# Kernel tuning notes

Hardware: AMD Instinct MI355X
Metric: run time of the kernel (lower is better)

The kernel has to match this reference:

```python
import jax, jax.numpy as jnp
import numpy as np

B = 8
IMG = 224; PATCH = 16; C_IN = 3
GRID = IMG // PATCH           # 14
NPATCH = GRID * GRID          # 196
D_MODEL = 768
N_LAYERS = 12
D_STATE = 16
D_CONV = 4
D_INNER = 2 * D_MODEL         # 1536
DT_RANK = 48                  # ceil(768/16)
MASK_RATIO = 0.25
LEN_KEEP = int(NPATCH * (1.0 - MASK_RATIO))  # 147


def _sincos_1d(dim, pos):
    omega = np.arange(dim // 2, dtype=np.float64) / (dim / 2.0)
    omega = 1.0 / (10000.0 ** omega)
    out = np.einsum('m,d->md', pos.reshape(-1).astype(np.float64), omega)
    return np.concatenate([np.sin(out), np.cos(out)], axis=1)


def get_2d_sincos_pos_embed(embed_dim, grid_size, add_cls_token=True):
    grid_h = np.arange(grid_size, dtype=np.float32)
    grid_w = np.arange(grid_size, dtype=np.float32)
    grid = np.meshgrid(grid_w, grid_h)
    grid = np.stack(grid, axis=0).reshape([2, 1, grid_size, grid_size])
    emb_h = _sincos_1d(embed_dim // 2, grid[0])
    emb_w = _sincos_1d(embed_dim // 2, grid[1])
    pos = np.concatenate([emb_h, emb_w], axis=1)
    if add_cls_token:
        pos = np.concatenate([np.zeros([1, embed_dim]), pos], axis=0)
    return pos.astype(np.float32)


def setup_inputs() -> dict:
    key = jax.random.key(0)
    ks = jax.random.split(key, 16)
    sc = 0.02
    pixel_values = jax.random.normal(ks[0], (B, C_IN, IMG, IMG), jnp.float32)
    noise = jax.random.uniform(ks[1], (B, NPATCH), jnp.float32)
    conv_w = jax.random.normal(ks[2], (D_MODEL, C_IN, PATCH, PATCH), jnp.float32) * sc
    conv_b = jnp.zeros((D_MODEL,), jnp.float32)
    cls_token = jax.random.normal(ks[3], (1, 1, D_MODEL), jnp.float32) * sc
    pos_embed = jnp.asarray(get_2d_sincos_pos_embed(D_MODEL, GRID, True))  # (197, 768)
    ln_w = jnp.ones((N_LAYERS, D_MODEL), jnp.float32)
    ln_b = jnp.zeros((N_LAYERS, D_MODEL), jnp.float32)
    W_in = jax.random.normal(ks[4], (N_LAYERS, 2 * D_INNER, D_MODEL), jnp.float32) * sc
    conv1d_w = jax.random.normal(ks[5], (N_LAYERS, D_INNER, D_CONV), jnp.float32) * sc
    conv1d_b = jnp.zeros((N_LAYERS, D_INNER), jnp.float32)
    W_x = jax.random.normal(ks[6], (N_LAYERS, DT_RANK + 2 * D_STATE, D_INNER), jnp.float32) * sc
    dt_std = DT_RANK ** (-0.5)
    W_dt = jax.random.uniform(ks[7], (N_LAYERS, D_INNER, DT_RANK), jnp.float32, -dt_std, dt_std)
    u = jax.random.uniform(ks[8], (N_LAYERS, D_INNER), jnp.float32)
    dt = jnp.exp(u * (np.log(0.1) - np.log(0.001)) + np.log(0.001))
    dt_bias = dt + jnp.log(-jnp.expm1(-dt))  # inverse softplus
    A_log = jnp.broadcast_to(jnp.log(jnp.arange(1, D_STATE + 1, dtype=jnp.float32)),
                             (N_LAYERS, D_INNER, D_STATE)).copy()
    Dp = jnp.ones((N_LAYERS, D_INNER), jnp.float32)
    W_out = jax.random.normal(ks[9], (N_LAYERS, D_MODEL, D_INNER), jnp.float32) * sc
    lnf_w = jnp.ones((D_MODEL,), jnp.float32)
    lnf_b = jnp.zeros((D_MODEL,), jnp.float32)
    return dict(pixel_values=pixel_values, noise=noise, conv_w=conv_w, conv_b=conv_b,
                cls_token=cls_token, pos_embed=pos_embed, ln_w=ln_w, ln_b=ln_b,
                W_in=W_in, conv1d_w=conv1d_w, conv1d_b=conv1d_b, W_x=W_x, W_dt=W_dt,
                dt_bias=dt_bias, A_log=A_log, Dp=Dp, W_out=W_out, lnf_w=lnf_w, lnf_b=lnf_b)


def layer_norm(x, w, b, eps=1e-12):
    mu = jnp.mean(x, axis=-1, keepdims=True)
    var = jnp.var(x, axis=-1, keepdims=True)
    return (x - mu) * jax.lax.rsqrt(var + eps) * w + b


def mamba_mixer(x, W_in, cw, cb, W_x, W_dt, dtb, A_log, Dp, W_out):
    # x: (B, L, D_MODEL)
    Bb, L, _ = x.shape
    xz = jnp.einsum('bld,ed->ble', x, W_in)           # (B, L, 2*d_inner)
    xs, z = jnp.split(xz, 2, axis=-1)
    # depthwise causal conv over time
    xc = xs.transpose(0, 2, 1)                        # (B, d_inner, L)
    xc = jax.lax.conv_general_dilated(xc, cw[:, None, :], (1,), [(D_CONV - 1, 0)],
                                      dimension_numbers=('NCH', 'OIH', 'NCH'),
                                      feature_group_count=D_INNER) + cb[None, :, None]
    xc = jax.nn.silu(xc).transpose(0, 2, 1)           # (B, L, d_inner)
    x_dbl = jnp.einsum('bld,rd->blr', xc, W_x)        # (B, L, dt_rank+2*d_state)
    dt, Bm, Cm = jnp.split(x_dbl, [DT_RANK, DT_RANK + D_STATE], axis=-1)
    dt = jax.nn.softplus(jnp.einsum('blr,dr->bld', dt, W_dt) + dtb)  # (B, L, d_inner)
    A = -jnp.exp(A_log)                               # (d_inner, d_state)
    dA = jnp.exp(dt[..., None] * A)                   # (B, L, d_inner, d_state)
    dBu = (dt * xc)[..., None] * Bm[:, :, None, :]    # (B, L, d_inner, d_state)

    def step(h, inp):
        dA_t, dBu_t, C_t = inp
        h = dA_t * h + dBu_t                          # (B, d_inner, d_state)
        y = jnp.einsum('bdn,bn->bd', h, C_t)
        return h, y

    h0 = jnp.zeros((Bb, D_INNER, D_STATE), xc.dtype)
    _, ys = jax.lax.scan(step, h0, (dA.transpose(1, 0, 2, 3), dBu.transpose(1, 0, 2, 3),
                                    Cm.transpose(1, 0, 2)))
    y = ys.transpose(1, 0, 2) + xc * Dp               # skip via D
    y = y * jax.nn.silu(z)                            # output gate
    return jnp.einsum('bld,od->blo', y, W_out)


def reference(pixel_values, noise, conv_w, conv_b, cls_token, pos_embed, ln_w, ln_b,
              W_in, conv1d_w, conv1d_b, W_x, W_dt, dt_bias, A_log, Dp, W_out, lnf_w, lnf_b):
    Bb = pixel_values.shape[0]
    # patch embedding (conv stride = patch)
    x = jax.lax.conv_general_dilated(pixel_values, conv_w, (PATCH, PATCH), 'VALID',
                                     dimension_numbers=('NCHW', 'OIHW', 'NCHW'))
    x = x.reshape(Bb, D_MODEL, NPATCH).transpose(0, 2, 1) + conv_b  # (B, 196, 768)
    x = x + pos_embed[1:][None]
    # random masking (noise supplied externally for determinism)
    ids_shuffle = jnp.argsort(noise, axis=1)
    ids_restore = jnp.argsort(ids_shuffle, axis=1)
    ids_keep = ids_shuffle[:, :LEN_KEEP]
    x = jnp.take_along_axis(x, ids_keep[:, :, None], axis=1)        # (B, 147, 768)
    mask = jnp.ones((Bb, NPATCH), jnp.float32).at[:, :LEN_KEEP].set(0.0)
    mask = jnp.take_along_axis(mask, ids_restore, axis=1)
    # prepend CLS
    cls = jnp.broadcast_to(cls_token + pos_embed[:1][None], (Bb, 1, D_MODEL))
    h = jnp.concatenate([cls, x], axis=1)                            # (B, 148, 768)

    def layer(hc, p):
        lw, lb, Wi, cw, cb, Wx, Wd, db, Al, Dd, Wo = p
        return hc + mamba_mixer(layer_norm(hc, lw, lb), Wi, cw, cb, Wx, Wd, db, Al, Dd, Wo), None

    h, _ = jax.lax.scan(layer, h, (ln_w, ln_b, W_in, conv1d_w, conv1d_b, W_x, W_dt,
                                   dt_bias, A_log, Dp, W_out))
    h = layer_norm(h, lnf_w, lnf_b)
    return h, mask, ids_restore
```

## Files before the change

### kernel.cpp

```cpp
#include <hip/hip_runtime.h>


#define BATCH 8
#define NPATCH 196
#define LEN_KEEP 147
#define SEQ 148
#define DM 768
#define DI 1536
#define DTR 48
#define DST 16
#define MTOK (BATCH*SEQ)
#define MT MTOK

typedef __bf16 bf16_t;
typedef bf16_t bf16x8 __attribute__((ext_vector_type(8)));
typedef float  f32x4  __attribute__((ext_vector_type(4)));
typedef unsigned short u16;
typedef u16 u16x8 __attribute__((ext_vector_type(8)));

__device__ __forceinline__ u16 f2bf(float f) {
    union { float f; unsigned u; } c; c.f = f;
    unsigned r = c.u + 0x7FFFu + ((c.u >> 16) & 1u);
    return (u16)(r >> 16);
}
__device__ __forceinline__ float bf2f(u16 u) {
    union { unsigned u; float f; } c; c.u = ((unsigned)u) << 16; return c.f;
}
__device__ __forceinline__ float sigmoidf_(float x) { return 1.f / (1.f + __expf(-x)); }

__device__ __forceinline__ void gl_lds16(const void* g, void* l) {
    __builtin_amdgcn_global_load_lds(
        (const __attribute__((address_space(1))) unsigned int*)g,
        (__attribute__((address_space(3))) unsigned int*)l, 16, 0, 0);
}

__global__ __launch_bounds__(256) void k_im2col(const float* __restrict__ px,
                                                u16* __restrict__ Ap) {
    int idx = blockIdx.x * 256 + threadIdx.x;
    if (idx >= 1568 * 192) return;
    int m = idx / 192, kq = (idx % 192) * 4;
    int b = m / NPATCH, p = m % NPATCH;
    int c = kq / 256, r = kq % 256, i = r / 16, j = r % 16;
    int y = (p / 14) * 16 + i, x = (p % 14) * 16 + j;
    float4 v = *reinterpret_cast<const float4*>(&px[((size_t)(b * 3 + c) * 224 + y) * 224 + x]);
    ushort4 w4 = { f2bf(v.x), f2bf(v.y), f2bf(v.z), f2bf(v.w) };
    *reinterpret_cast<ushort4*>(&Ap[(size_t)m * 768 + kq]) = w4;
}

__global__ __launch_bounds__(256) void k_mask(const float* __restrict__ noise,
                                              int* __restrict__ ids_shuf,
                                              float* __restrict__ out_mask,
                                              float* __restrict__ out_restore) {
    __shared__ float sn[NPATCH];
    __shared__ int sshuf[NPATCH];
    int b = blockIdx.x, tid = threadIdx.x;
    if (tid < NPATCH) sn[tid] = noise[b * NPATCH + tid];
    __syncthreads();
    if (tid < NPATCH) {
        float nj = sn[tid];
        int rank = 0;
        for (int i = 0; i < NPATCH; ++i) {
            float ni = sn[i];
            rank += (ni < nj) || (ni == nj && i < tid);
        }
        out_restore[b * NPATCH + tid] = (float)rank;
        out_mask[b * NPATCH + tid] = (rank >= LEN_KEEP) ? 1.f : 0.f;
        sshuf[rank] = tid;
    }
    __syncthreads();
    if (tid < NPATCH) ids_shuf[b * NPATCH + tid] = sshuf[tid];
}

__global__ __launch_bounds__(256) void k_build_h(const float* __restrict__ embed,
                                                 const int* __restrict__ ids_shuf,
                                                 const float* __restrict__ cls,
                                                 const float* __restrict__ pos,
                                                 float* __restrict__ h) {
    int blk = blockIdx.x;
    int b = blk / SEQ, t = blk % SEQ, tid = threadIdx.x;
    size_t ob = (size_t)blk * DM;
    if (t == 0) {
        for (int i = tid; i < DM; i += 256) h[ob + i] = cls[i] + pos[i];
    } else {
        int j = ids_shuf[b * NPATCH + (t - 1)];
        const float* src = embed + (size_t)(b * NPATCH + j) * DM;
        for (int i = tid; i < DM; i += 256) h[ob + i] = src[i];
    }
}

template <int OUT_BF>
__global__ __launch_bounds__(256) void k_layernorm(const float* __restrict__ in,
                                                   const float* __restrict__ w,
                                                   const float* __restrict__ b,
                                                   void* __restrict__ outv) {
    int row = blockIdx.x, tid = threadIdx.x;
    const float* x = in + (size_t)row * DM;
    float v0 = x[tid], v1 = x[tid + 256], v2 = x[tid + 512];
    float s = v0 + v1 + v2, q = v0 * v0 + v1 * v1 + v2 * v2;
#pragma unroll
    for (int off = 32; off; off >>= 1) {
        s += __shfl_down(s, off, 64);
        q += __shfl_down(q, off, 64);
    }
    __shared__ float ss[4], sq[4];
    int wid = tid >> 6, lane = tid & 63;
    if (lane == 0) { ss[wid] = s; sq[wid] = q; }
    __syncthreads();
    float st = ss[0] + ss[1] + ss[2] + ss[3];
    float qt = sq[0] + sq[1] + sq[2] + sq[3];
    float mu = st * (1.f / DM);
    float var = qt * (1.f / DM) - mu * mu;
    float rstd = rsqrtf(var + 1e-12f);
    float r0 = (v0 - mu) * rstd * w[tid]       + b[tid];
    float r1 = (v1 - mu) * rstd * w[tid + 256] + b[tid + 256];
    float r2 = (v2 - mu) * rstd * w[tid + 512] + b[tid + 512];
    if (OUT_BF) {
        u16* o = (u16*)outv + (size_t)row * DM;
        o[tid] = f2bf(r0); o[tid + 256] = f2bf(r1); o[tid + 512] = f2bf(r2);
    } else {
        float* o = (float*)outv + (size_t)row * DM;
        o[tid] = r0; o[tid + 256] = r1; o[tid + 512] = r2;
    }
}

template <int EPI>
__global__ __launch_bounds__(256) void gemm64(
    const u16* __restrict__ A, int lda, int M,
    const u16* __restrict__ B, int ldb, int N,
    void* __restrict__ Cv, int ldc, int kChunk,
    const float* __restrict__ e0, const float* __restrict__ e1) {
    __shared__ u16 sm[2][128 * 64];
    const int tid = threadIdx.x;
    const int m0 = blockIdx.x * 64, n0 = blockIdx.y * 64;
    const int kStart = blockIdx.z * kChunk;
    const int lane = tid & 63, wid = tid >> 6;
    const int wr = wid >> 1, wc = wid & 1;
    const int lr = lane & 15, lg = lane >> 4;
    const int subrow = lane >> 3, kpart = lane & 7;
    const int kel = 8 * (kpart ^ subrow);

    f32x4 acc[2][2] = {};
    const int nt = kChunk / 64;

    {
        const int k0 = kStart;
#pragma unroll
        for (int s = 0; s < 2; ++s) {
            int rb = wid * 16 + s * 8;
            int ra = min(m0 + rb + subrow, M - 1);
            gl_lds16(A + (size_t)ra * lda + k0 + kel, &sm[0][rb * 64]);
            int rn = min(n0 + rb + subrow, N - 1);
            gl_lds16(B + (size_t)rn * ldb + k0 + kel, &sm[0][64 * 64 + rb * 64]);
        }
    }
    __syncthreads();
    for (int t = 0; t < nt; ++t) {
        if (t + 1 < nt) {
            const int k0 = kStart + (t + 1) * 64;
            const int buf = (t + 1) & 1;
#pragma unroll
            for (int s = 0; s < 2; ++s) {
                int rb = wid * 16 + s * 8;
                int ra = min(m0 + rb + subrow, M - 1);
                gl_lds16(A + (size_t)ra * lda + k0 + kel, &sm[buf][rb * 64]);
                int rn = min(n0 + rb + subrow, N - 1);
                gl_lds16(B + (size_t)rn * ldb + k0 + kel, &sm[buf][64 * 64 + rb * 64]);
            }
        }
        {
            const u16* sA = &sm[t & 1][0];
            const u16* sB = &sm[t & 1][64 * 64];
#pragma unroll
            for (int kk = 0; kk < 2; ++kk) {
                bf16x8 av[2], bv[2];
#pragma unroll
                for (int i = 0; i < 2; ++i) {
                    int row = wr * 32 + i * 16 + lr;
                    int e = (kk * 32 + lg * 8) ^ ((row & 7) << 3);
                    av[i] = *reinterpret_cast<const bf16x8*>(sA + row * 64 + e);
                }
#pragma unroll
                for (int j = 0; j < 2; ++j) {
                    int row = wc * 32 + j * 16 + lr;
                    int e = (kk * 32 + lg * 8) ^ ((row & 7) << 3);
                    bv[j] = *reinterpret_cast<const bf16x8*>(sB + row * 64 + e);
                }
#pragma unroll
                for (int i = 0; i < 2; ++i)
#pragma unroll
                    for (int j = 0; j < 2; ++j)
                        acc[i][j] = __builtin_amdgcn_mfma_f32_16x16x32_bf16(
                            av[i], bv[j], acc[i][j], 0, 0, 0);
            }
        }
        __syncthreads();
    }
#pragma unroll
    for (int i = 0; i < 2; ++i)
#pragma unroll
        for (int r = 0; r < 4; ++r) {
            int m = m0 + wr * 32 + i * 16 + lg * 4 + r;
            if (m >= M) continue;
#pragma unroll
            for (int j = 0; j < 2; ++j) {
                int n = n0 + wc * 32 + j * 16 + lr;
                if (n >= N) continue;
                float v = acc[i][j][r];
                size_t idx = (size_t)m * ldc + n;
                if (EPI == 1) {
                    atomicAdd((float*)Cv + idx, v);
                } else if (EPI == 2) {
                    ((float*)Cv)[idx] = v + e0[n] + e1[(size_t)(1 + (m % NPATCH)) * DM + n];
                } else if (EPI == 3) {
                    float x = v + e0[n];
                    ((u16*)Cv)[idx] = f2bf(x > 20.f ? x : log1pf(__expf(x)));
                } else if (EPI == 4) {
                    ((u16*)Cv)[idx] = f2bf(v);
                } else {
                    float x = v + e0[m];
                    ((u16*)Cv)[idx] = f2bf(x > 20.f ? x : log1pf(__expf(x)));
                }
            }
        }
}

template <int TC>
__device__ __forceinline__ void conv_piece(const u16* __restrict__ xrow,
                                           const float w0, const float w1,
                                           const float w2, const float w3,
                                           const float cbv,
                                           u16* __restrict__ sout) {
    constexpr int START = (TC == 0) ? 0 : (TC == 1) ? 32 : (TC == 2) ? 64 : 104;
    u16x8 buf[6];
#pragma unroll
    for (int i = 0; i < 6; ++i)
        buf[i] = *reinterpret_cast<const u16x8*>(xrow + START + 8 * i);
    const float wj[4] = { w0, w1, w2, w3 };
#pragma unroll
    for (int i = 0; i < 37; ++i) {
        const int t = TC * 37 + i;
        float acc = cbv;
#pragma unroll
        for (int j = 0; j < 4; ++j) {
            const int q = t - 3 + j;
            if (TC == 0 && q < 0) continue;
            const int idx = q - START;
            acc += bf2f(buf[idx >> 3][idx & 7]) * wj[j];
        }
        acc = acc * sigmoidf_(acc);
        sout[t] = f2bf(acc);
    }
}

__global__ __launch_bounds__(256) void k_conv(
    const u16* __restrict__ xzT,
    const float* __restrict__ cw,
    const float* __restrict__ cb,
    u16* __restrict__ xcT,
    u16* __restrict__ xcTok,
    float* __restrict__ xdbl) {
    __shared__ u16 sxc[64][152];
    const int tid = threadIdx.x;
    const int d0 = blockIdx.x * 64, b = blockIdx.y;
    const int dl = tid & 63, tc = tid >> 6;
    const int d = d0 + dl;
    float4 w4 = *reinterpret_cast<const float4*>(&cw[d * 4]);
    float cbv = cb[d];
    const u16* xrow = xzT + (size_t)d * MT + b * SEQ;
    switch (tc) {
        case 0: conv_piece<0>(xrow, w4.x, w4.y, w4.z, w4.w, cbv, &sxc[dl][0]); break;
        case 1: conv_piece<1>(xrow, w4.x, w4.y, w4.z, w4.w, cbv, &sxc[dl][0]); break;
        case 2: conv_piece<2>(xrow, w4.x, w4.y, w4.z, w4.w, cbv, &sxc[dl][0]); break;
        default: conv_piece<3>(xrow, w4.x, w4.y, w4.z, w4.w, cbv, &sxc[dl][0]); break;
    }
    if (blockIdx.x == 0) {
        float4* xo = reinterpret_cast<float4*>(xdbl + (size_t)b * SEQ * 80);
        for (int c = tid; c < SEQ * 20; c += 256) xo[c] = make_float4(0.f, 0.f, 0.f, 0.f);
    }
    __syncthreads();
    for (int c = tid; c < 64 * 19; c += 256) {
        int dd = c / 19, ch = c % 19;
        size_t gbase = (size_t)(d0 + dd) * MT + b * SEQ;
        if (ch < 18)
            *reinterpret_cast<u16x8*>(&xcT[gbase + ch * 8]) =
                *reinterpret_cast<const u16x8*>(&sxc[dd][ch * 8]);
        else
            *reinterpret_cast<ushort4*>(&xcT[gbase + 144]) =
                *reinterpret_cast<const ushort4*>(&sxc[dd][144]);
    }
    if (tid < SEQ) {
        int t = tid;
        size_t gb = (size_t)(b * SEQ + t) * DI + d0;
#pragma unroll
        for (int g = 0; g < 8; ++g) {
            u16x8 v;
#pragma unroll
            for (int e = 0; e < 8; ++e) v[e] = sxc[g * 8 + e][t];
            *reinterpret_cast<u16x8*>(&xcTok[gb + g * 8]) = v;
        }
    }
}

__global__ __launch_bounds__(256) void k_scan(
    const u16* __restrict__ dtT,
    const u16* __restrict__ xcT,
    const u16* __restrict__ xzT,
    const float* __restrict__ xdT,
    const float* __restrict__ A_log,
    const float* __restrict__ Dp,
    u16* __restrict__ y) {
    __shared__ u16 sy[16][152];
    const int tid = threadIdx.x;
    const int d0 = blockIdx.x * 16, b = blockIdx.y;
    const int dl = tid >> 4, n = tid & 15;
    const int d = d0 + dl;
    const float An = -__expf(A_log[d * DST + n]);
    const float Dv = Dp[d];
    const u16* dtrow = dtT + (size_t)d * MT + b * SEQ;
    const u16* xcrow = xcT + (size_t)d * MT + b * SEQ;
    const u16* zrow  = xzT + (size_t)(DI + d) * MT + b * SEQ;
    const float* Brow = xdT + (size_t)n * MT + b * SEQ;
    const float* Crow = xdT + (size_t)(16 + n) * MT + b * SEQ;
    float h = 0.f;
    for (int t0 = 0; t0 < SEQ; t0 += 8) {
        u16x8 dt8 = *reinterpret_cast<const u16x8*>(dtrow + t0);
        u16x8 xc8 = *reinterpret_cast<const u16x8*>(xcrow + t0);
        u16x8 z8  = *reinterpret_cast<const u16x8*>(zrow + t0);
        float4 B0 = *reinterpret_cast<const float4*>(Brow + t0);
        float4 B1 = *reinterpret_cast<const float4*>(Brow + t0 + 4);
        float4 C0 = *reinterpret_cast<const float4*>(Crow + t0);
        float4 C1 = *reinterpret_cast<const float4*>(Crow + t0 + 4);
        const float Ba[8] = { B0.x, B0.y, B0.z, B0.w, B1.x, B1.y, B1.z, B1.w };
        const float Ca[8] = { C0.x, C0.y, C0.z, C0.w, C1.x, C1.y, C1.z, C1.w };
#pragma unroll
        for (int j = 0; j < 8; ++j) {
            if (t0 + j < SEQ) {
                float dtv = bf2f(dt8[j]);
                float xcv = bf2f(xc8[j]);
                float e = __expf(dtv * An);
                h = e * h + (dtv * xcv) * Ba[j];
                float yp = h * Ca[j];
                yp += __shfl_xor(yp, 1, 64);
                yp += __shfl_xor(yp, 2, 64);
                yp += __shfl_xor(yp, 4, 64);
                yp += __shfl_xor(yp, 8, 64);
                if (n == 0) {
                    float zv = bf2f(z8[j]);
                    sy[dl][t0 + j] = f2bf((yp + xcv * Dv) * (zv * sigmoidf_(zv)));
                }
            }
        }
    }
    __syncthreads();
    if (tid < SEQ) {
        int t = tid;
        size_t gb = (size_t)(b * SEQ + t) * DI + d0;
#pragma unroll
        for (int g = 0; g < 2; ++g) {
            u16x8 v;
#pragma unroll
            for (int e = 0; e < 8; ++e) v[e] = sy[g * 8 + e][t];
            *reinterpret_cast<u16x8*>(&y[gb + g * 8]) = v;
        }
    }
}

__global__ __launch_bounds__(256) void k_cvt(const float* __restrict__ s,
                                             u16* __restrict__ d, int n4) {
    int i = blockIdx.x * 256 + threadIdx.x;
    if (i >= n4) return;
    float4 v = *reinterpret_cast<const float4*>(s + (size_t)i * 4);
    ushort4 w4 = { f2bf(v.x), f2bf(v.y), f2bf(v.z), f2bf(v.w) };
    *reinterpret_cast<ushort4*>(d + (size_t)i * 4) = w4;
}

#define WS0 2359296
#define WS1 1179648
#define WS2 122880
#define WS3 98304
__global__ __launch_bounds__(256) void k_cvtw(
    const float* __restrict__ Wi, const float* __restrict__ Wo,
    const float* __restrict__ Wx, const float* __restrict__ Wd,
    u16* __restrict__ oi, u16* __restrict__ oo,
    u16* __restrict__ ox, u16* __restrict__ od) {
    long i4 = ((long)blockIdx.x * 256 + threadIdx.x) * 4;
    if (i4 < WS0) {
        float4 v = *reinterpret_cast<const float4*>(Wi + i4);
        ushort4 w4 = { f2bf(v.x), f2bf(v.y), f2bf(v.z), f2bf(v.w) };
        *reinterpret_cast<ushort4*>(oi + i4) = w4;
    } else if (i4 < WS0 + WS1) {
        long j = i4 - WS0;
        float4 v = *reinterpret_cast<const float4*>(Wo + j);
        ushort4 w4 = { f2bf(v.x), f2bf(v.y), f2bf(v.z), f2bf(v.w) };
        *reinterpret_cast<ushort4*>(oo + j) = w4;
    } else if (i4 < WS0 + WS1 + WS2) {
        long j = i4 - WS0 - WS1;
        float4 v = *reinterpret_cast<const float4*>(Wx + j);
        ushort4 w4 = { f2bf(v.x), f2bf(v.y), f2bf(v.z), f2bf(v.w) };
        *reinterpret_cast<ushort4*>(ox + j) = w4;
    } else if (i4 < WS0 + WS1 + WS2 + WS3) {
        long j = i4 - WS0 - WS1 - WS2;
        int rw = (int)(j >> 6), c = (int)(j & 63);
        ushort4 w4 = { 0, 0, 0, 0 };
        if (c < DTR) {
            float4 v = *reinterpret_cast<const float4*>(Wd + (size_t)rw * DTR + c);
            w4 = { f2bf(v.x), f2bf(v.y), f2bf(v.z), f2bf(v.w) };
        }
        *reinterpret_cast<ushort4*>(od + j) = w4;
    }
}

__global__ __launch_bounds__(256) void k_cvt_xdbl(const float* __restrict__ x,
                                                  u16* __restrict__ obf,
                                                  float* __restrict__ oT) {
    int i = blockIdx.x * 256 + threadIdx.x;
    if (i < MTOK * 64) {
        int r = i >> 6, c = i & 63;
        obf[i] = (c < DTR) ? f2bf(x[(size_t)r * 80 + c]) : (u16)0;
    } else {
        int j = i - MTOK * 64;
        if (j < 32 * MTOK) {
            int rr = j / MTOK, m = j - rr * MTOK;
            oT[(size_t)rr * MTOK + m] = x[(size_t)m * 80 + 48 + rr];
        }
    }
}

extern "C" void kernel_launch(void* const* d_in, const int* in_sizes, int n_in,
                              void* d_out, int out_size, void* d_ws, size_t ws_size,
                              hipStream_t stream) {
    const float* pixel  = (const float*)d_in[0];
    const float* noise  = (const float*)d_in[1];
    const float* conv_w = (const float*)d_in[2];
    const float* conv_b = (const float*)d_in[3];
    const float* cls    = (const float*)d_in[4];
    const float* pos    = (const float*)d_in[5];
    const float* ln_w   = (const float*)d_in[6];
    const float* ln_b   = (const float*)d_in[7];
    const float* W_in   = (const float*)d_in[8];
    const float* c1w    = (const float*)d_in[9];
    const float* c1b    = (const float*)d_in[10];
    const float* W_x    = (const float*)d_in[11];
    const float* W_dt   = (const float*)d_in[12];
    const float* dtb    = (const float*)d_in[13];
    const float* A_log  = (const float*)d_in[14];
    const float* Dp     = (const float*)d_in[15];
    const float* W_out  = (const float*)d_in[16];
    const float* lnf_w  = (const float*)d_in[17];
    const float* lnf_b  = (const float*)d_in[18];

    float* out = (float*)d_out;
    float* h = out;
    float* out_mask    = out + MTOK * DM;
    float* out_restore = out + MTOK * DM + BATCH * NPATCH;

    char* wsb = (char*)d_ws;
    u16*  xzT     = (u16*)(wsb + 0);
    u16*  xcT     = (u16*)(wsb + 7274560);
    u16*  xcTok   = (u16*)(wsb + 10911872);
    u16*  dtT     = (u16*)(wsb + 14549120);
    u16*  yb      = (u16*)(wsb + 18186432);
    u16*  xln_bf  = (u16*)(wsb + 21823680);
    float* xdbl   = (float*)(wsb + 23642304);
    u16*  xdbl_bf = (u16*)(wsb + 24021184);
    float* xdT    = (float*)(wsb + 24172736);
    u16*  apatch  = (u16*)(wsb + 24324352);
    float* embed  = (float*)(wsb + 26732800);
    int*  ids     = (int*)(wsb + 31549696);
    u16*  cw_bf   = (u16*)(wsb + 31555968);
    u16*  wi_bf   = (u16*)(wsb + 32735616);
    u16*  wo_bf   = wi_bf + WS0;
    u16*  wx_bf   = wo_bf + WS1;
    u16*  wd_bf   = wx_bf + WS2;

    k_im2col<<<1176, 256, 0, stream>>>(pixel, apatch);
    k_mask<<<BATCH, 256, 0, stream>>>(noise, ids, out_mask, out_restore);
    k_cvt<<<576, 256, 0, stream>>>(conv_w, cw_bf, 147456);
    gemm64<2><<<dim3(25, 12, 1), 256, 0, stream>>>(
        apatch, 768, 1568, cw_bf, 768, 768, embed, DM, 768, conv_b, pos);
    k_build_h<<<MTOK, 256, 0, stream>>>(embed, ids, cls, pos, h);

    for (int l = 0; l < 12; ++l) {
        k_cvtw<<<3672, 256, 0, stream>>>(
            W_in + (size_t)l * WS0, W_out + (size_t)l * WS1,
            W_x + (size_t)l * WS2, W_dt + (size_t)l * DI * DTR,
            wi_bf, wo_bf, wx_bf, wd_bf);
        k_layernorm<1><<<MTOK, 256, 0, stream>>>(h, ln_w + l * DM, ln_b + l * DM, xln_bf);
        gemm64<4><<<dim3(48, 19, 1), 256, 0, stream>>>(
            wi_bf, DM, 3072, xln_bf, DM, MTOK, xzT, MT, DM, nullptr, nullptr);
        k_conv<<<dim3(24, 8), 256, 0, stream>>>(
            xzT, c1w + l * DI * 4, c1b + l * DI, xcT, xcTok, xdbl);
        gemm64<1><<<dim3(19, 2, 8), 256, 0, stream>>>(
            xcTok, DI, MTOK, wx_bf, DI, 80, xdbl, 80, 192, nullptr, nullptr);
        k_cvt_xdbl<<<444, 256, 0, stream>>>(xdbl, xdbl_bf, xdT);
        gemm64<5><<<dim3(24, 19, 1), 256, 0, stream>>>(
            wd_bf, 64, DI, xdbl_bf, 64, MTOK, dtT, MT, 64, dtb + l * DI, nullptr);
        k_scan<<<dim3(96, 8), 256, 0, stream>>>(
            dtT, xcT, xzT, xdT, A_log + (size_t)l * DI * DST, Dp + l * DI, yb);
        gemm64<1><<<dim3(19, 12, 2), 256, 0, stream>>>(
            yb, DI, MTOK, wo_bf, DI, DM, h, DM, 768, nullptr, nullptr);
    }
    k_layernorm<0><<<MTOK, 256, 0, stream>>>(h, lnf_w, lnf_b, h);
}
```

Before: 1.568 ms.

## Batch weight conversion into one launch and use 128x128 GEMM tiles for in/out projections

Replaces the per-layer weight fp32-to-bf16 conversion kernel with a single upfront kernel that converts all 12 layers' weights into a larger workspace. This removes 12 launches and their serialization. Adds a 128x128-tile MFMA GEMM with double-buffered LDS staging, used for the in-projection and the split-K out-projection, to raise data reuse per block. The larger workspace and the lower block counts (240 blocks) could hurt occupancy and CU coverage.

New measurement: 1.624 ms. +3.6%, slower.

```diff
diff --git a/kernel.cpp b/kernel.cpp
--- a/kernel.cpp
+++ b/kernel.cpp
@@ -220,6 +220,86 @@
                     float x = v + e0[m];
                     ((u16*)Cv)[idx] = f2bf(x > 20.f ? x : log1pf(__expf(x)));
                 }
+            }
+        }
+}
+
+template <int EPI>
+__global__ __launch_bounds__(256) void gemm128(
+    const u16* __restrict__ A, int lda, int M,
+    const u16* __restrict__ B, int ldb, int N,
+    void* __restrict__ Cv, int ldc, int kChunk) {
+    __shared__ u16 sm[2][2 * 128 * 64];
+    const int tid = threadIdx.x;
+    const int m0 = blockIdx.x * 128, n0 = blockIdx.y * 128;
+    const int kStart = blockIdx.z * kChunk;
+    const int lane = tid & 63, wid = tid >> 6;
+    const int wr = wid >> 1, wc = wid & 1;
+    const int lr = lane & 15, lg = lane >> 4;
+    const int subrow = lane >> 3, kpart = lane & 7;
+    const int kel = 8 * (kpart ^ subrow);
+
+    f32x4 acc[4][4] = {};
+    const int nt = kChunk / 64;
+
+#define STAGE128(buf, k0)                                                     \
+    {                                                                         \
+        _Pragma("unroll")                                                     \
+        for (int s = 0; s < 4; ++s) {                                         \
+            int rb = wid * 32 + s * 8;                                        \
+            int ra = min(m0 + rb + subrow, M - 1);                            \
+            gl_lds16(A + (size_t)ra * lda + (k0) + kel, &sm[buf][rb * 64]);   \
+            int rn = min(n0 + rb + subrow, N - 1);                            \
+            gl_lds16(B + (size_t)rn * ldb + (k0) + kel,                       \
+                     &sm[buf][128 * 64 + rb * 64]);                           \
+        }                                                                     \
+    }
+
+    STAGE128(0, kStart);
+    __syncthreads();
+    for (int t = 0; t < nt; ++t) {
+        if (t + 1 < nt) STAGE128((t + 1) & 1, kStart + (t + 1) * 64);
+        const u16* sA = &sm[t & 1][0];
+        const u16* sB = &sm[t & 1][128 * 64];
+#pragma unroll
+        for (int kk = 0; kk < 2; ++kk) {
+            bf16x8 av[4], bv[4];
+#pragma unroll
+            for (int i = 0; i < 4; ++i) {
+                int row = wr * 64 + i * 16 + lr;
+                int e = (kk * 32 + lg * 8) ^ ((row & 7) << 3);
+                av[i] = *reinterpret_cast<const bf16x8*>(sA + row * 64 + e);
+            }
+#pragma unroll
+            for (int j = 0; j < 4; ++j) {
+                int row = wc * 64 + j * 16 + lr;
+                int e = (kk * 32 + lg * 8) ^ ((row & 7) << 3);
+                bv[j] = *reinterpret_cast<const bf16x8*>(sB + row * 64 + e);
+            }
+#pragma unroll
+            for (int i = 0; i < 4; ++i)
+#pragma unroll
+                for (int j = 0; j < 4; ++j)
+                    acc[i][j] = __builtin_amdgcn_mfma_f32_16x16x32_bf16(
+                        av[i], bv[j], acc[i][j], 0, 0, 0);
+        }
+        __syncthreads();
+    }
+#undef STAGE128
+#pragma unroll
+    for (int i = 0; i < 4; ++i)
+#pragma unroll
+        for (int r = 0; r < 4; ++r) {
+            int m = m0 + wr * 64 + i * 16 + lg * 4 + r;
+            if (m >= M) continue;
+#pragma unroll
+            for (int j = 0; j < 4; ++j) {
+                int n = n0 + wc * 64 + j * 16 + lr;
+                if (n >= N) continue;
+                float v = acc[i][j][r];
+                size_t idx = (size_t)m * ldc + n;
+                if (EPI == 1) atomicAdd((float*)Cv + idx, v);
+                else          ((u16*)Cv)[idx] = f2bf(v);
             }
         }
 }
@@ -374,39 +454,43 @@
     *reinterpret_cast<ushort4*>(d + (size_t)i * 4) = w4;
 }
 
-#define WS0 2359296
-#define WS1 1179648
-#define WS2 122880
-#define WS3 98304
-__global__ __launch_bounds__(256) void k_cvtw(
+#define QWI 7077888L
+#define QWO 3538944L
+#define QWX 368640L
+#define QWD 294912L
+__global__ __launch_bounds__(256) void k_cvtw_all(
     const float* __restrict__ Wi, const float* __restrict__ Wo,
     const float* __restrict__ Wx, const float* __restrict__ Wd,
     u16* __restrict__ oi, u16* __restrict__ oo,
     u16* __restrict__ ox, u16* __restrict__ od) {
-    long i4 = ((long)blockIdx.x * 256 + threadIdx.x) * 4;
-    if (i4 < WS0) {
-        float4 v = *reinterpret_cast<const float4*>(Wi + i4);
+    long q = (long)blockIdx.x * 256 + threadIdx.x;
+    if (q < QWI) {
+        long e = q * 4;
+        float4 v = *reinterpret_cast<const float4*>(Wi + e);
         ushort4 w4 = { f2bf(v.x), f2bf(v.y), f2bf(v.z), f2bf(v.w) };
-        *reinterpret_cast<ushort4*>(oi + i4) = w4;
-    } else if (i4 < WS0 + WS1) {
-        long j = i4 - WS0;
-        float4 v = *reinterpret_cast<const float4*>(Wo + j);
+        *reinterpret_cast<ushort4*>(oi + e) = w4;
+    } else if (q < QWI + QWO) {
+        long e = (q - QWI) * 4;
+        float4 v = *reinterpret_cast<const float4*>(Wo + e);
         ushort4 w4 = { f2bf(v.x), f2bf(v.y), f2bf(v.z), f2bf(v.w) };
-        *reinterpret_cast<ushort4*>(oo + j) = w4;
-    } else if (i4 < WS0 + WS1 + WS2) {
-        long j = i4 - WS0 - WS1;
-        float4 v = *reinterpret_cast<const float4*>(Wx + j);
+        *reinterpret_cast<ushort4*>(oo + e) = w4;
+    } else if (q < QWI + QWO + QWX) {
+        long e = (q - QWI - QWO) * 4;
+        float4 v = *reinterpret_cast<const float4*>(Wx + e);
         ushort4 w4 = { f2bf(v.x), f2bf(v.y), f2bf(v.z), f2bf(v.w) };
-        *reinterpret_cast<ushort4*>(ox + j) = w4;
-    } else if (i4 < WS0 + WS1 + WS2 + WS3) {
-        long j = i4 - WS0 - WS1 - WS2;
-        int rw = (int)(j >> 6), c = (int)(j & 63);
+        *reinterpret_cast<ushort4*>(ox + e) = w4;
+    } else {
+        long e = (q - QWI - QWO - QWX) * 4;
+        int l = (int)(e / 98304);
+        int rem = (int)(e % 98304);
+        int rw = rem >> 6, c = rem & 63;
         ushort4 w4 = { 0, 0, 0, 0 };
         if (c < DTR) {
-            float4 v = *reinterpret_cast<const float4*>(Wd + (size_t)rw * DTR + c);
+            float4 v = *reinterpret_cast<const float4*>(
+                Wd + (size_t)l * (DI * DTR) + (size_t)rw * DTR + c);
             w4 = { f2bf(v.x), f2bf(v.y), f2bf(v.z), f2bf(v.w) };
         }
-        *reinterpret_cast<ushort4*>(od + j) = w4;
+        *reinterpret_cast<ushort4*>(od + e) = w4;
     }
 }
 
@@ -467,38 +551,40 @@
     u16*  apatch  = (u16*)(wsb + 24324352);
     float* embed  = (float*)(wsb + 26732800);
     int*  ids     = (int*)(wsb + 31549696);
-    u16*  cw_bf   = (u16*)(wsb + 31555968);
-    u16*  wi_bf   = (u16*)(wsb + 32735616);
-    u16*  wo_bf   = wi_bf + WS0;
-    u16*  wx_bf   = wo_bf + WS1;
-    u16*  wd_bf   = wx_bf + WS2;
+    u16*  cw_bf   = (u16*)(wsb + 31556032);
+    u16*  wi_all  = (u16*)(wsb + 32735680);
+    u16*  wo_all  = wi_all + QWI * 4;
+    u16*  wx_all  = wo_all + QWO * 4;
+    u16*  wd_all  = wx_all + QWX * 4;
 
     k_im2col<<<1176, 256, 0, stream>>>(pixel, apatch);
     k_mask<<<BATCH, 256, 0, stream>>>(noise, ids, out_mask, out_restore);
     k_cvt<<<576, 256, 0, stream>>>(conv_w, cw_bf, 147456);
+    k_cvtw_all<<<44064, 256, 0, stream>>>(W_in, W_out, W_x, W_dt,
+                                          wi_all, wo_all, wx_all, wd_all);
     gemm64<2><<<dim3(25, 12, 1), 256, 0, stream>>>(
         apatch, 768, 1568, cw_bf, 768, 768, embed, DM, 768, conv_b, pos);
     k_build_h<<<MTOK, 256, 0, stream>>>(embed, ids, cls, pos, h);
 
     for (int l = 0; l < 12; ++l) {
-        k_cvtw<<<3672, 256, 0, stream>>>(
-            W_in + (size_t)l * WS0, W_out + (size_t)l * WS1,
-            W_x + (size_t)l * WS2, W_dt + (size_t)l * DI * DTR,
-            wi_bf, wo_bf, wx_bf, wd_bf);
+        const u16* wi = wi_all + (size_t)l * 2359296;
+        const u16* wo = wo_all + (size_t)l * 1179648;
+        const u16* wx = wx_all + (size_t)l * 122880;
+        const u16* wd = wd_all + (size_t)l * 98304;
         k_layernorm<1><<<MTOK, 256, 0, stream>>>(h, ln_w + l * DM, ln_b + l * DM, xln_bf);
-        gemm64<4><<<dim3(48, 19, 1), 256, 0, stream>>>(
-            wi_bf, DM, 3072, xln_bf, DM, MTOK, xzT, MT, DM, nullptr, nullptr);
+        gemm128<4><<<dim3(24, 10, 1), 256, 0, stream>>>(
+            wi, DM, 3072, xln_bf, DM, MTOK, xzT, MT, DM);
         k_conv<<<dim3(24, 8), 256, 0, stream>>>(
             xzT, c1w + l * DI * 4, c1b + l * DI, xcT, xcTok, xdbl);
         gemm64<1><<<dim3(19, 2, 8), 256, 0, stream>>>(
-            xcTok, DI, MTOK, wx_bf, DI, 80, xdbl, 80, 192, nullptr, nullptr);
+            xcTok, DI, MTOK, wx, DI, 80, xdbl, 80, 192, nullptr, nullptr);
         k_cvt_xdbl<<<444, 256, 0, stream>>>(xdbl, xdbl_bf, xdT);
         gemm64<5><<<dim3(24, 19, 1), 256, 0, stream>>>(
-            wd_bf, 64, DI, xdbl_bf, 64, MTOK, dtT, MT, 64, dtb + l * DI, nullptr);
+            wd, 64, DI, xdbl_bf, 64, MTOK, dtT, MT, 64, dtb + l * DI, nullptr);
         k_scan<<<dim3(96, 8), 256, 0, stream>>>(
             dtT, xcT, xzT, xdT, A_log + (size_t)l * DI * DST, Dp + l * DI, yb);
-        gemm64<1><<<dim3(19, 12, 2), 256, 0, stream>>>(
-            yb, DI, MTOK, wo_bf, DI, DM, h, DM, 768, nullptr, nullptr);
+        gemm128<1><<<dim3(10, 6, 4), 256, 0, stream>>>(
+            yb, DI, MTOK, wo, DI, DM, h, DM, 384);
     }
     k_layernorm<0><<<MTOK, 256, 0, stream>>>(h, lnf_w, lnf_b, h);
 }
```

## Hoist weight conversion out of layer loop and fuse xdbl conversion into consumers

Applied to the files above, without the earlier changes.

Converts all layers' weights (plus the patch conv weight) to bf16 in one up-front launch instead of one conversion kernel per layer. A dedicated dt-projection GEMM reads fp32 xdbl directly, converting it to bf16 while staging into LDS, and applies bias plus softplus. The scan kernel stages B/C from xdbl into shared memory itself. Together these remove the k_cvt_xdbl launch and its transposed intermediate. It costs a much larger workspace holding all layers' bf16 weights and a serialised LDS staging phase at the start of the scan.

After: 1.495 ms. 4.7% less time.

```diff
diff --git a/kernel.cpp b/kernel.cpp
--- a/kernel.cpp
+++ b/kernel.cpp
@@ -211,15 +211,84 @@
                     atomicAdd((float*)Cv + idx, v);
                 } else if (EPI == 2) {
                     ((float*)Cv)[idx] = v + e0[n] + e1[(size_t)(1 + (m % NPATCH)) * DM + n];
-                } else if (EPI == 3) {
-                    float x = v + e0[n];
-                    ((u16*)Cv)[idx] = f2bf(x > 20.f ? x : log1pf(__expf(x)));
-                } else if (EPI == 4) {
+                } else {
                     ((u16*)Cv)[idx] = f2bf(v);
-                } else {
-                    float x = v + e0[m];
-                    ((u16*)Cv)[idx] = f2bf(x > 20.f ? x : log1pf(__expf(x)));
                 }
+            }
+        }
+}
+
+__global__ __launch_bounds__(256) void gemm_dtf(
+    const u16* __restrict__ A,
+    const float* __restrict__ Bx,
+    const float* __restrict__ dtb,
+    u16* __restrict__ dtT) {
+    __shared__ u16 sA[64 * 64];
+    __shared__ u16 sB[64 * 64];
+    const int tid = threadIdx.x;
+    const int m0 = blockIdx.x * 64, n0 = blockIdx.y * 64;
+    const int lane = tid & 63, wid = tid >> 6;
+    const int wr = wid >> 1, wc = wid & 1;
+    const int lr = lane & 15, lg = lane >> 4;
+    const int subrow = lane >> 3, kpart = lane & 7;
+    const int kel = 8 * (kpart ^ subrow);
+#pragma unroll
+    for (int s = 0; s < 2; ++s) {
+        int rb = wid * 16 + s * 8;
+        gl_lds16(A + (size_t)(m0 + rb + subrow) * 64 + kel, &sA[rb * 64]);
+    }
+    {
+        int r = tid >> 2, g0 = (tid & 3) * 2;
+        int rn = min(n0 + r, MTOK - 1);
+#pragma unroll
+        for (int gi = 0; gi < 2; ++gi) {
+            int g = g0 + gi;
+            u16x8 w = { 0, 0, 0, 0, 0, 0, 0, 0 };
+            if (g < 6) {
+                float4 a = *reinterpret_cast<const float4*>(Bx + (size_t)rn * 80 + g * 8);
+                float4 c = *reinterpret_cast<const float4*>(Bx + (size_t)rn * 80 + g * 8 + 4);
+                w[0] = f2bf(a.x); w[1] = f2bf(a.y); w[2] = f2bf(a.z); w[3] = f2bf(a.w);
+                w[4] = f2bf(c.x); w[5] = f2bf(c.y); w[6] = f2bf(c.z); w[7] = f2bf(c.w);
+            }
+            *reinterpret_cast<u16x8*>(&sB[r * 64 + ((g ^ (r & 7)) * 8)]) = w;
+        }
+    }
+    __syncthreads();
+    f32x4 acc[2][2] = {};
+#pragma unroll
+    for (int kk = 0; kk < 2; ++kk) {
+        bf16x8 av[2], bv[2];
+#pragma unroll
+        for (int i = 0; i < 2; ++i) {
+            int row = wr * 32 + i * 16 + lr;
+            int e = (kk * 32 + lg * 8) ^ ((row & 7) << 3);
+            av[i] = *reinterpret_cast<const bf16x8*>(sA + row * 64 + e);
+        }
+#pragma unroll
+        for (int j = 0; j < 2; ++j) {
+            int row = wc * 32 + j * 16 + lr;
+            int e = (kk * 32 + lg * 8) ^ ((row & 7) << 3);
+            bv[j] = *reinterpret_cast<const bf16x8*>(sB + row * 64 + e);
+        }
+#pragma unroll
+        for (int i = 0; i < 2; ++i)
+#pragma unroll
+            for (int j = 0; j < 2; ++j)
+                acc[i][j] = __builtin_amdgcn_mfma_f32_16x16x32_bf16(
+                    av[i], bv[j], acc[i][j], 0, 0, 0);
+    }
+#pragma unroll
+    for (int i = 0; i < 2; ++i)
+#pragma unroll
+        for (int r = 0; r < 4; ++r) {
+            int m = m0 + wr * 32 + i * 16 + lg * 4 + r;
+            float bias = dtb[m];
+#pragma unroll
+            for (int j = 0; j < 2; ++j) {
+                int n = n0 + wc * 32 + j * 16 + lr;
+                if (n >= MTOK) continue;
+                float x = acc[i][j][r] + bias;
+                dtT[(size_t)m * MT + n] = f2bf(x > 20.f ? x : log1pf(__expf(x)));
             }
         }
 }
@@ -305,41 +374,39 @@
     const u16* __restrict__ dtT,
     const u16* __restrict__ xcT,
     const u16* __restrict__ xzT,
-    const float* __restrict__ xdT,
+    const float* __restrict__ xdbl,
     const float* __restrict__ A_log,
     const float* __restrict__ Dp,
     u16* __restrict__ y) {
+    __shared__ float sBC[32][149];
     __shared__ u16 sy[16][152];
     const int tid = threadIdx.x;
     const int d0 = blockIdx.x * 16, b = blockIdx.y;
     const int dl = tid >> 4, n = tid & 15;
     const int d = d0 + dl;
+    for (int i = tid; i < 32 * SEQ; i += 256) {
+        int t = i >> 5, c = i & 31;
+        sBC[c][t] = xdbl[(size_t)(b * SEQ + t) * 80 + 48 + c];
+    }
     const float An = -__expf(A_log[d * DST + n]);
     const float Dv = Dp[d];
     const u16* dtrow = dtT + (size_t)d * MT + b * SEQ;
     const u16* xcrow = xcT + (size_t)d * MT + b * SEQ;
     const u16* zrow  = xzT + (size_t)(DI + d) * MT + b * SEQ;
-    const float* Brow = xdT + (size_t)n * MT + b * SEQ;
-    const float* Crow = xdT + (size_t)(16 + n) * MT + b * SEQ;
     float h = 0.f;
+    __syncthreads();
     for (int t0 = 0; t0 < SEQ; t0 += 8) {
         u16x8 dt8 = *reinterpret_cast<const u16x8*>(dtrow + t0);
         u16x8 xc8 = *reinterpret_cast<const u16x8*>(xcrow + t0);
         u16x8 z8  = *reinterpret_cast<const u16x8*>(zrow + t0);
-        float4 B0 = *reinterpret_cast<const float4*>(Brow + t0);
-        float4 B1 = *reinterpret_cast<const float4*>(Brow + t0 + 4);
-        float4 C0 = *reinterpret_cast<const float4*>(Crow + t0);
-        float4 C1 = *reinterpret_cast<const float4*>(Crow + t0 + 4);
-        const float Ba[8] = { B0.x, B0.y, B0.z, B0.w, B1.x, B1.y, B1.z, B1.w };
-        const float Ca[8] = { C0.x, C0.y, C0.z, C0.w, C1.x, C1.y, C1.z, C1.w };
 #pragma unroll
         for (int j = 0; j < 8; ++j) {
             if (t0 + j < SEQ) {
                 float dtv = bf2f(dt8[j]);
                 float xcv = bf2f(xc8[j]);
                 float e = __expf(dtv * An);
-                h = e * h + (dtv * xcv) * Ba[j];
-                float yp = h * Ca[j];
+                h = e * h + (dtv * xcv) * sBC[n][t0 + j];
+                float yp = h * sBC[16 + n][t0 + j];
                 yp += __shfl_xor(yp, 1, 64);
                 yp += __shfl_xor(yp, 2, 64);
                 yp += __shfl_xor(yp, 4, 64);
@@ -365,65 +432,47 @@
     }
 }
 
-__global__ __launch_bounds__(256) void k_cvt(const float* __restrict__ s,
-                                             u16* __restrict__ d, int n4) {
-    int i = blockIdx.x * 256 + threadIdx.x;
-    if (i >= n4) return;
-    float4 v = *reinterpret_cast<const float4*>(s + (size_t)i * 4);
-    ushort4 w4 = { f2bf(v.x), f2bf(v.y), f2bf(v.z), f2bf(v.w) };
-    *reinterpret_cast<ushort4*>(d + (size_t)i * 4) = w4;
-}
-
-#define WS0 2359296
-#define WS1 1179648
-#define WS2 122880
-#define WS3 98304
-__global__ __launch_bounds__(256) void k_cvtw(
-    const float* __restrict__ Wi, const float* __restrict__ Wo,
-    const float* __restrict__ Wx, const float* __restrict__ Wd,
-    u16* __restrict__ oi, u16* __restrict__ oo,
+#define PCW 73728
+#define PWI 3538944
+#define PWO 1769472
+#define PWX 184320
+#define PWD 147456
+__global__ __launch_bounds__(256) void k_cvtw_all(
+    const float* __restrict__ cwsrc, const float* __restrict__ Wi,
+    const float* __restrict__ Wo, const float* __restrict__ Wx,
+    const float* __restrict__ Wd,
+    u16* __restrict__ ocw, u16* __restrict__ oi, u16* __restrict__ oo,
     u16* __restrict__ ox, u16* __restrict__ od) {
-    long i4 = ((long)blockIdx.x * 256 + threadIdx.x) * 4;
-    if (i4 < WS0) {
-        float4 v = *reinterpret_cast<const float4*>(Wi + i4);
-        ushort4 w4 = { f2bf(v.x), f2bf(v.y), f2bf(v.z), f2bf(v.w) };
-        *reinterpret_cast<ushort4*>(oi + i4) = w4;
-    } else if (i4 < WS0 + WS1) {
-        long j = i4 - WS0;
-        float4 v = *reinterpret_cast<const float4*>(Wo + j);
-        ushort4 w4 = { f2bf(v.x), f2bf(v.y), f2bf(v.z), f2bf(v.w) };
-        *reinterpret_cast<ushort4*>(oo + j) = w4;
-    } else if (i4 < WS0 + WS1 + WS2) {
-        long j = i4 - WS0 - WS1;
-        float4 v = *reinterpret_cast<const float4*>(Wx + j);
-        ushort4 w4 = { f2bf(v.x), f2bf(v.y), f2bf(v.z), f2bf(v.w) };
-        *reinterpret_cast<ushort4*>(ox + j) = w4;
-    } else if (i4 < WS0 + WS1 + WS2 + WS3) {
-        long j = i4 - WS0 - WS1 - WS2;
-        int rw = (int)(j >> 6), c = (int)(j & 63);
-        ushort4 w4 = { 0, 0, 0, 0 };
-        if (c < DTR) {
-            float4 v = *reinterpret_cast<const float4*>(Wd + (size_t)rw * DTR + c);
-            w4 = { f2bf(v.x), f2bf(v.y), f2bf(v.z), f2bf(v.w) };
-        }
-        *reinterpret_cast<ushort4*>(od + j) = w4;
-    }
-}
-
-__global__ __launch_bounds__(256) void k_cvt_xdbl(const float* __restrict__ x,
-                                                  u16* __restrict__ obf,
-                                                  float* __restrict__ oT) {
-    int i = blockIdx.x * 256 + threadIdx.x;
-    if (i < MTOK * 64) {
-        int r = i >> 6, c = i & 63;
-        obf[i] = (c < DTR) ? f2bf(x[(size_t)r * 80 + c]) : (u16)0;
+    int p = blockIdx.x * 256 + threadIdx.x;
+    const float* src;
+    u16* dst;
+    bool zero_hi = false;
+    if (p < PCW) {
+        src = cwsrc + (size_t)p * 8; dst = ocw + (size_t)p * 8;
+    } else if (p < PCW + PWI) {
+        size_t e = (size_t)(p - PCW) * 8; src = Wi + e; dst = oi + e;
+    } else if (p < PCW + PWI + PWO) {
+        size_t e = (size_t)(p - PCW - PWI) * 8; src = Wo + e; dst = oo + e;
+    } else if (p < PCW + PWI + PWO + PWX) {
+        size_t e = (size_t)(p - PCW - PWI - PWO) * 8; src = Wx + e; dst = ox + e;
     } else {
-        int j = i - MTOK * 64;
-        if (j < 32 * MTOK) {
-            int rr = j / MTOK, m = j - rr * MTOK;
-            oT[(size_t)rr * MTOK + m] = x[(size_t)m * 80 + 48 + rr];
-        }
-    }
+        int q = p - PCW - PWI - PWO - PWX;
+        int ei = q * 8;
+        int rw = ei >> 6, c0 = ei & 63;
+        dst = od + ei;
+        if (c0 < DTR) { src = Wd + (size_t)rw * DTR + c0; }
+        else { src = Wd; zero_hi = true; }
+    }
+    u16x8 w;
+    if (zero_hi) {
+        w = (u16x8){ 0, 0, 0, 0, 0, 0, 0, 0 };
+    } else {
+        float4 a = *reinterpret_cast<const float4*>(src);
+        float4 c = *reinterpret_cast<const float4*>(src + 4);
+        w[0] = f2bf(a.x); w[1] = f2bf(a.y); w[2] = f2bf(a.z); w[3] = f2bf(a.w);
+        w[4] = f2bf(c.x); w[5] = f2bf(c.y); w[6] = f2bf(c.z); w[7] = f2bf(c.w);
+    }
+    *reinterpret_cast<u16x8*>(dst) = w;
 }
 
 extern "C" void kernel_launch(void* const* d_in, const int* in_sizes, int n_in,
@@ -462,43 +511,40 @@
     u16*  yb      = (u16*)(wsb + 18186432);
     u16*  xln_bf  = (u16*)(wsb + 21823680);
     float* xdbl   = (float*)(wsb + 23642304);
-    u16*  xdbl_bf = (u16*)(wsb + 24021184);
-    float* xdT    = (float*)(wsb + 24172736);
-    u16*  apatch  = (u16*)(wsb + 24324352);
-    float* embed  = (float*)(wsb + 26732800);
-    int*  ids     = (int*)(wsb + 31549696);
-    u16*  cw_bf   = (u16*)(wsb + 31555968);
-    u16*  wi_bf   = (u16*)(wsb + 32735616);
-    u16*  wo_bf   = wi_bf + WS0;
-    u16*  wx_bf   = wo_bf + WS1;
-    u16*  wd_bf   = wx_bf + WS2;
+    u16*  apatch  = (u16*)(wsb + 24021184);
+    float* embed  = (float*)(wsb + 26429632);
+    int*  ids     = (int*)(wsb + 31246528);
+    u16*  cw_bf   = (u16*)(wsb + 31252864);
+    u16*  wi_all  = (u16*)(wsb + 32432512);
+    u16*  wo_all  = wi_all + 28311552;
+    u16*  wx_all  = wo_all + 14155776;
+    u16*  wd_all  = wx_all + 1474560;
 
     k_im2col<<<1176, 256, 0, stream>>>(pixel, apatch);
     k_mask<<<BATCH, 256, 0, stream>>>(noise, ids, out_mask, out_restore);
-    k_cvt<<<576, 256, 0, stream>>>(conv_w, cw_bf, 147456);
+    k_cvtw_all<<<22320, 256, 0, stream>>>(conv_w, W_in, W_out, W_x, W_dt,
+                                          cw_bf, wi_all, wo_all, wx_all, wd_all);
     gemm64<2><<<dim3(25, 12, 1), 256, 0, stream>>>(
         apatch, 768, 1568, cw_bf, 768, 768, embed, DM, 768, conv_b, pos);
     k_build_h<<<MTOK, 256, 0, stream>>>(embed, ids, cls, pos, h);
 
     for (int l = 0; l < 12; ++l) {
-        k_cvtw<<<3672, 256, 0, stream>>>(
-            W_in + (size_t)l * WS0, W_out + (size_t)l * WS1,
-            W_x + (size_t)l * WS2, W_dt + (size_t)l * DI * DTR,
-            wi_bf, wo_bf, wx_bf, wd_bf);
+        const u16* wi = wi_all + (size_t)l * 2359296;
+        const u16* wo = wo_all + (size_t)l * 1179648;
+        const u16* wx = wx_all + (size_t)l * 122880;
+        const u16* wd = wd_all + (size_t)l * 98304;
         k_layernorm<1><<<MTOK, 256, 0, stream>>>(h, ln_w + l * DM, ln_b + l * DM, xln_bf);
         gemm64<4><<<dim3(48, 19, 1), 256, 0, stream>>>(
-            wi_bf, DM, 3072, xln_bf, DM, MTOK, xzT, MT, DM, nullptr, nullptr);
+            wi, DM, 3072, xln_bf, DM, MTOK, xzT, MT, DM, nullptr, nullptr);
         k_conv<<<dim3(24, 8), 256, 0, stream>>>(
             xzT, c1w + l * DI * 4, c1b + l * DI, xcT, xcTok, xdbl);
         gemm64<1><<<dim3(19, 2, 8), 256, 0, stream>>>(
-            xcTok, DI, MTOK, wx_bf, DI, 80, xdbl, 80, 192, nullptr, nullptr);
-        k_cvt_xdbl<<<444, 256, 0, stream>>>(xdbl, xdbl_bf, xdT);
-        gemm64<5><<<dim3(24, 19, 1), 256, 0, stream>>>(
-            wd_bf, 64, DI, xdbl_bf, 64, MTOK, dtT, MT, 64, dtb + l * DI, nullptr);
+            xcTok, DI, MTOK, wx, DI, 80, xdbl, 80, 192, nullptr, nullptr);
+        gemm_dtf<<<dim3(24, 19), 256, 0, stream>>>(wd, xdbl, dtb + l * DI, dtT);
         k_scan<<<dim3(96, 8), 256, 0, stream>>>(
-            dtT, xcT, xzT, xdT, A_log + (size_t)l * DI * DST, Dp + l * DI, yb);
+            dtT, xcT, xzT, xdbl, A_log + (size_t)l * DI * DST, Dp + l * DI, yb);
         gemm64<1><<<dim3(19, 12, 2), 256, 0, stream>>>(
-            yb, DI, MTOK, wo_bf, DI, DM, h, DM, 768, nullptr, nullptr);
+            yb, DI, MTOK, wo, DI, DM, h, DM, 768, nullptr, nullptr);
     }
     k_layernorm<0><<<MTOK, 256, 0, stream>>>(h, lnf_w, lnf_b, h);
 }
```
